# Kernel optimization log

Measured on AMD Instinct MI355X. Metric: run time of the kernel, lower is better.

The kernel has to match this reference:

```python
import jax, jax.numpy as jnp
import numpy as np

N_NODES = 50000
N_EDGES = 800000
NODE_F = 128
EDGE_F = 64
OUT_F = 128


def setup_inputs() -> dict:
    key = jax.random.key(0)
    k1, k2, k3, k4, k5 = jax.random.split(key, 5)
    x = jax.random.normal(k1, (N_NODES, NODE_F), dtype=jnp.float32)
    edge_index = jax.random.randint(k2, (2, N_EDGES), 0, N_NODES, dtype=jnp.int64)
    edge_attr = jax.random.normal(k3, (N_EDGES, EDGE_F), dtype=jnp.float32)
    # Linear(node_features + edge_features, out_features) params (torch default init scale)
    fan_in = NODE_F + EDGE_F
    bound = 1.0 / np.sqrt(fan_in)
    W = jax.random.uniform(k4, (fan_in, OUT_F), minval=-bound, maxval=bound, dtype=jnp.float32)
    b = jax.random.uniform(k5, (OUT_F,), minval=-bound, maxval=bound, dtype=jnp.float32)
    return {"x": x, "edge_index": edge_index, "edge_attr": edge_attr, "W": W, "b": b}


def reference(x, edge_index, edge_attr, W, b):
    # PyG source_to_target flow: x_j = x[src], aggregate at dst
    src = edge_index[0]
    dst = edge_index[1]
    x_j = x[src]                                   # [E, node_f] gather
    feats = jnp.concatenate([edge_attr, x_j], axis=1)  # [E, edge_f + node_f]
    msg = jax.nn.relu(feats @ W + b)               # [E, out_f] Linear + ReLU
    out = jax.ops.segment_sum(msg, dst, num_segments=x.shape[0])  # scatter-add
    return out
```

## Files before the change

kernel.cpp:

```cpp
#include <hip/hip_runtime.h>
#include <hip/hip_bf16.h>

#define N_NODES 50000
#define N_EDGES 800000
#define NODE_F  128
#define EDGE_F  64
#define OUT_F   128

#define NCH ((N_NODES + 255) / 256)
#define EPW 128
#define NRANGES (N_EDGES / EPW)

typedef __attribute__((ext_vector_type(8))) short short8;
typedef __attribute__((ext_vector_type(4))) short short4v;
typedef __attribute__((ext_vector_type(4))) float floatx4;

__device__ __forceinline__ unsigned short f2bf(float f) {
    unsigned int u = __float_as_uint(f);
    u += 0x7fffu + ((u >> 16) & 1u);
    return (unsigned short)(u >> 16);
}

__device__ __forceinline__ short8 cvt8(floatx4 v0, floatx4 v1) {
    union { __hip_bfloat162 h[4]; short8 s; } u;
    u.h[0] = __float22bfloat162_rn(make_float2(v0[0], v0[1]));
    u.h[1] = __float22bfloat162_rn(make_float2(v0[2], v0[3]));
    u.h[2] = __float22bfloat162_rn(make_float2(v1[0], v1[1]));
    u.h[3] = __float22bfloat162_rn(make_float2(v1[2], v1[3]));
    return u.s;
}

#define TILE_N1 32
#define N_NTILES ((N_NODES + TILE_N1 - 1) / TILE_N1)
#define LDS_STRIDE1 136

__global__ __launch_bounds__(256, 4) void node_kernel(
    const float* __restrict__ x,
    const float* __restrict__ W,
    const float* __restrict__ bias,
    float*       __restrict__ Y)
{
    __shared__ __align__(16) unsigned short xs[TILE_N1][LDS_STRIDE1];

    const int tid  = threadIdx.x;
    const int wave = tid >> 6;
    const int lane = tid & 63;
    const int col  = lane & 15;
    const int quad = lane >> 4;
    const int wbase = wave * 32;

    const float* __restrict__ Wx = W + EDGE_F * OUT_F;

    short8 bfr[4][2];
    #pragma unroll
    for (int kc = 0; kc < 4; ++kc) {
        #pragma unroll
        for (int ns = 0; ns < 2; ++ns) {
            const int n = wbase + ns * 16 + col;
            const int krow = kc * 32 + quad * 8;
            short8 v;
            #pragma unroll
            for (int j = 0; j < 8; ++j)
                v[j] = (short)f2bf(Wx[(krow + j) * OUT_F + n]);
            bfr[kc][ns] = v;
        }
    }
    const float b0 = bias[wbase + col];
    const float b1 = bias[wbase + 16 + col];

    for (int tile = blockIdx.x; tile < N_NTILES; tile += gridDim.x) {
        const int n0 = tile * TILE_N1;
        {
            const int e   = tid >> 3;
            const int sub = tid & 7;
            const int node = n0 + e;
            const float* __restrict__ xr = x + (size_t)node * NODE_F;
            #pragma unroll
            for (int i = 0; i < 4; ++i) {
                const int fi = sub + 8 * i;
                floatx4 v = {0.f, 0.f, 0.f, 0.f};
                if (node < N_NODES) v = *(const floatx4*)(xr + fi * 4);
                union { __hip_bfloat162 h[2]; short4v s; } u;
                u.h[0] = __float22bfloat162_rn(make_float2(v[0], v[1]));
                u.h[1] = __float22bfloat162_rn(make_float2(v[2], v[3]));
                *(short4v*)&xs[e][fi * 4] = u.s;
            }
        }
        __syncthreads();

        floatx4 acc[2][2] = {};
        #pragma unroll
        for (int kc = 0; kc < 4; ++kc) {
            short8 a0 = *(const short8*)&xs[col     ][kc * 32 + quad * 8];
            short8 a1 = *(const short8*)&xs[16 + col][kc * 32 + quad * 8];
            acc[0][0] = __builtin_amdgcn_mfma_f32_16x16x32_bf16(a0, bfr[kc][0], acc[0][0], 0, 0, 0);
            acc[0][1] = __builtin_amdgcn_mfma_f32_16x16x32_bf16(a0, bfr[kc][1], acc[0][1], 0, 0, 0);
            acc[1][0] = __builtin_amdgcn_mfma_f32_16x16x32_bf16(a1, bfr[kc][0], acc[1][0], 0, 0, 0);
            acc[1][1] = __builtin_amdgcn_mfma_f32_16x16x32_bf16(a1, bfr[kc][1], acc[1][1], 0, 0, 0);
        }

        #pragma unroll
        for (int ms = 0; ms < 2; ++ms) {
            #pragma unroll
            for (int r = 0; r < 4; ++r) {
                const int m = ms * 16 + quad * 4 + r;
                const int node = n0 + m;
                if (node < N_NODES) {
                    float* yrow = Y + (size_t)node * OUT_F + wbase;
                    yrow[col]      = acc[ms][0][r] + b0;
                    yrow[16 + col] = acc[ms][1][r] + b1;
                }
            }
        }
        __syncthreads();
    }
}

__global__ void hist_kernel(const int* __restrict__ edge_index, int* __restrict__ hist) {
    const int* dstp = edge_index + N_EDGES;
    for (int i = blockIdx.x * blockDim.x + threadIdx.x; i < N_EDGES;
         i += gridDim.x * blockDim.x)
        atomicAdd(&hist[dstp[i]], 1);
}

__global__ void scan1_kernel(const int* __restrict__ hist, int* __restrict__ chunkSum) {
    __shared__ int s[256];
    const int c = blockIdx.x, t = threadIdx.x, idx = c * 256 + t;
    s[t] = (idx < N_NODES) ? hist[idx] : 0;
    __syncthreads();
    for (int off = 128; off > 0; off >>= 1) {
        if (t < off) s[t] += s[t + off];
        __syncthreads();
    }
    if (t == 0) chunkSum[c] = s[0];
}

__global__ void scan2_kernel(const int* __restrict__ chunkSum, int* __restrict__ chunkBase) {
    __shared__ int s[256];
    const int t = threadIdx.x;
    s[t] = (t < NCH) ? chunkSum[t] : 0;
    __syncthreads();
    for (int off = 1; off < 256; off <<= 1) {
        int u = (t >= off) ? s[t - off] : 0;
        __syncthreads();
        s[t] += u;
        __syncthreads();
    }
    if (t < NCH) chunkBase[t] = (t == 0) ? 0 : s[t - 1];
}

__global__ void scan3_kernel(const int* __restrict__ hist, const int* __restrict__ chunkBase,
                             int* __restrict__ row_off, int* __restrict__ cursor) {
    __shared__ int s[256];
    const int c = blockIdx.x, t = threadIdx.x, idx = c * 256 + t;
    const int v = (idx < N_NODES) ? hist[idx] : 0;
    s[t] = v;
    __syncthreads();
    for (int off = 1; off < 256; off <<= 1) {
        int u = (t >= off) ? s[t - off] : 0;
        __syncthreads();
        s[t] += u;
        __syncthreads();
    }
    const int excl = s[t] - v + chunkBase[c];
    if (idx < N_NODES) { row_off[idx] = excl; cursor[idx] = excl; }
    if (c == 0 && t == 0) row_off[N_NODES] = N_EDGES;
}

__device__ __forceinline__ int lbound(const int* __restrict__ ro, int target) {
    int lo = 0, hi = N_NODES;
    while (lo < hi) {
        const int mid = (lo + hi) >> 1;
        if (ro[mid] < target) lo = mid + 1; else hi = mid;
    }
    return lo;
}

__global__ void range_kernel(const int* __restrict__ row_off, int* __restrict__ range_start) {
    const int rg = blockIdx.x * blockDim.x + threadIdx.x;
    if (rg <= NRANGES) range_start[rg] = row_off[lbound(row_off, rg * EPW)];
}

__global__ void scatter_kernel(const int* __restrict__ edge_index,
                               int* __restrict__ cursor, int2* __restrict__ sorted) {
    const int* srcp = edge_index;
    const int* dstp = edge_index + N_EDGES;
    for (int i = blockIdx.x * blockDim.x + threadIdx.x; i < N_EDGES;
         i += gridDim.x * blockDim.x) {
        const int d = dstp[i];
        const int p = atomicAdd(&cursor[d], 1);
        sorted[p] = make_int2(i, (int)(((unsigned)srcp[i] << 16) | (unsigned)d));
    }
}

__global__ __launch_bounds__(256, 6) void edge_gemm(
    const float* __restrict__ edge_attr,
    const float* __restrict__ W,
    const float* __restrict__ Y,
    const int*   __restrict__ range_start,
    const int2*  __restrict__ sorted,
    float*       __restrict__ out)
{
    __shared__ float CT[4][16][68];

    const int tid  = threadIdx.x;
    const int wave = tid >> 6;
    const int lane = tid & 63;
    const int col  = lane & 15;
    const int quad = lane >> 4;
    const int p    = wave & 1;

    short8 bfr[2][4];
    #pragma unroll
    for (int kc = 0; kc < 2; ++kc) {
        #pragma unroll
        for (int ns = 0; ns < 4; ++ns) {
            const int n = p * 64 + ns * 16 + col;
            const int krow = kc * 32 + quad * 8;
            short8 v;
            #pragma unroll
            for (int j = 0; j < 8; ++j)
                v[j] = (short)f2bf(W[(krow + j) * OUT_F + n]);
            bfr[kc][ns] = v;
        }
    }

    float* __restrict__ obase = out + p * 64 + lane;

    const int grange = blockIdx.x * 2 + (wave >> 1);
    const int stride = gridDim.x * 2;

    for (int rg = grange; rg < NRANGES; rg += stride) {
        const int eb = range_start[rg];
        const int ee = range_start[rg + 1];
        if (eb >= ee) continue;

        int   cur = -1;
        float s   = 0.f;

        int2 me = sorted[min(eb + col, ee - 1)];
        short8 a[2];
        {
            const float* __restrict__ ar = edge_attr + (size_t)me.x * EDGE_F;
            #pragma unroll
            for (int kc = 0; kc < 2; ++kc)
                a[kc] = cvt8(*(const floatx4*)(ar + kc * 32 + quad * 8),
                             *(const floatx4*)(ar + kc * 32 + quad * 8 + 4));
        }

        for (int t0 = eb; t0 < ee; t0 += 16) {
            floatx4 acc[4];
            #pragma unroll
            for (int r = 0; r < 4; ++r) {
                const int src = (int)((unsigned)__shfl(me.y, quad * 4 + r) >> 16);
                const float* __restrict__ yr = Y + (size_t)src * OUT_F + p * 64;
                #pragma unroll
                for (int ns = 0; ns < 4; ++ns)
                    acc[ns][r] = yr[ns * 16 + col];
            }

            #pragma unroll
            for (int kc = 0; kc < 2; ++kc) {
                #pragma unroll
                for (int ns = 0; ns < 4; ++ns)
                    acc[ns] = __builtin_amdgcn_mfma_f32_16x16x32_bf16(a[kc], bfr[kc][ns], acc[ns], 0, 0, 0);
            }

            #pragma unroll
            for (int r = 0; r < 4; ++r) {
                const bool rvalid = (t0 + quad * 4 + r) < ee;
                #pragma unroll
                for (int ns = 0; ns < 4; ++ns)
                    CT[wave][quad * 4 + r][ns * 16 + col] =
                        rvalid ? fmaxf(acc[ns][r], 0.f) : 0.f;
            }
            __builtin_amdgcn_wave_barrier();

            const int t1 = t0 + 16;
            int2 me2;
            if (t1 < ee) me2 = sorted[min(t1 + col, ee - 1)];

            float cv[16];
            #pragma unroll
            for (int m = 0; m < 16; ++m) cv[m] = CT[wave][m][lane];

            const int mez = me.y;
            #pragma unroll
            for (int m = 0; m < 16; ++m) {
                const int d = (int)((unsigned)__builtin_amdgcn_readlane(mez, m) & 0xffffu);
                if (d != cur) {
                    if (cur >= 0) obase[(size_t)cur * OUT_F] = s;
                    cur = d; s = 0.f;
                }
                s += cv[m];
            }
            cur = __builtin_amdgcn_readfirstlane(cur);
            __builtin_amdgcn_wave_barrier();

            if (t1 < ee) {
                me = me2;
                const float* __restrict__ ar = edge_attr + (size_t)me.x * EDGE_F;
                #pragma unroll
                for (int kc = 0; kc < 2; ++kc)
                    a[kc] = cvt8(*(const floatx4*)(ar + kc * 32 + quad * 8),
                                 *(const floatx4*)(ar + kc * 32 + quad * 8 + 4));
            }
        }
        if (cur >= 0) obase[(size_t)cur * OUT_F] = s;
    }
}

__global__ __launch_bounds__(256, 3) void edge_kernel_atomic(
    const float* __restrict__ edge_attr,
    const int*   __restrict__ edge_index,
    const float* __restrict__ W,
    const float* __restrict__ Y,
    float*       __restrict__ out)
{
    const int lane = threadIdx.x & 63;
    const int col  = lane & 15;
    const int quad = lane >> 4;

    short8 bfr[2][8];
    #pragma unroll
    for (int kc = 0; kc < 2; ++kc)
        #pragma unroll
        for (int ns = 0; ns < 8; ++ns) {
            const int n = ns * 16 + col;
            const int krow = kc * 32 + quad * 8;
            short8 v;
            #pragma unroll
            for (int j = 0; j < 8; ++j)
                v[j] = (short)f2bf(W[(krow + j) * OUT_F + n]);
            bfr[kc][ns] = v;
        }

    const int* __restrict__ srcp = edge_index;
    const int* __restrict__ dstp = edge_index + N_EDGES;

    const int gwave  = blockIdx.x * 4 + (threadIdx.x >> 6);
    const int nwaves = gridDim.x * 4;

    for (int t = gwave; t < N_EDGES / 16; t += nwaves) {
        const int e0 = t * 16;
        const float* __restrict__ ar = edge_attr + (size_t)(e0 + col) * EDGE_F;
        short8 a[2];
        #pragma unroll
        for (int kc = 0; kc < 2; ++kc)
            a[kc] = cvt8(*(const floatx4*)(ar + kc * 32 + quad * 8),
                         *(const floatx4*)(ar + kc * 32 + quad * 8 + 4));
        int sr[4], dr[4];
        #pragma unroll
        for (int r = 0; r < 4; ++r) {
            sr[r] = srcp[e0 + quad * 4 + r];
            dr[r] = dstp[e0 + quad * 4 + r];
        }
        floatx4 acc[8];
        #pragma unroll
        for (int ns = 0; ns < 8; ++ns)
            #pragma unroll
            for (int r = 0; r < 4; ++r)
                acc[ns][r] = Y[(size_t)sr[r] * OUT_F + ns * 16 + col];
        #pragma unroll
        for (int kc = 0; kc < 2; ++kc)
            #pragma unroll
            for (int ns = 0; ns < 8; ++ns)
                acc[ns] = __builtin_amdgcn_mfma_f32_16x16x32_bf16(a[kc], bfr[kc][ns], acc[ns], 0, 0, 0);
        #pragma unroll
        for (int ns = 0; ns < 8; ++ns)
            #pragma unroll
            for (int r = 0; r < 4; ++r) {
                const float v = acc[ns][r];
                if (v > 0.0f)
                    atomicAdd(out + (size_t)dr[r] * OUT_F + ns * 16 + col, v);
            }
    }
}

extern "C" void kernel_launch(void* const* d_in, const int* in_sizes, int n_in,
                              void* d_out, int out_size, void* d_ws, size_t ws_size,
                              hipStream_t stream) {
    const float* x          = (const float*)d_in[0];
    const int*   edge_index = (const int*)  d_in[1];
    const float* edge_attr  = (const float*)d_in[2];
    const float* W          = (const float*)d_in[3];
    const float* bias       = (const float*)d_in[4];
    float*       out        = (float*)d_out;

    float* Y          = (float*)d_ws;
    int2*  sorted     = (int2*)(Y + (size_t)N_NODES * OUT_F);
    int*   hist       = (int*)(sorted + N_EDGES);
    int*   chunkSum   = hist + N_NODES;
    int*   chunkBase  = chunkSum + 256;
    int*   row_off    = chunkBase + 256;
    int*   cursor     = row_off + N_NODES + 1;
    int*   range_start= cursor + N_NODES;
    const size_t needed = (size_t)((char*)(range_start + NRANGES + 1) - (char*)d_ws);

    hipMemsetAsync(out, 0, (size_t)out_size * sizeof(float), stream);
    node_kernel<<<dim3(512), dim3(256), 0, stream>>>(x, W, bias, Y);

    if (ws_size < needed) {
        edge_kernel_atomic<<<dim3(1024), dim3(256), 0, stream>>>(edge_attr, edge_index, W, Y, out);
        return;
    }

    hipMemsetAsync(hist, 0, (size_t)N_NODES * sizeof(int), stream);
    hist_kernel   <<<dim3(2048), dim3(256), 0, stream>>>(edge_index, hist);
    scan1_kernel  <<<dim3(NCH),  dim3(256), 0, stream>>>(hist, chunkSum);
    scan2_kernel  <<<dim3(1),    dim3(256), 0, stream>>>(chunkSum, chunkBase);
    scan3_kernel  <<<dim3(NCH),  dim3(256), 0, stream>>>(hist, chunkBase, row_off, cursor);
    range_kernel  <<<dim3((NRANGES + 256) / 256), dim3(256), 0, stream>>>(row_off, range_start);
    scatter_kernel<<<dim3(2048), dim3(256), 0, stream>>>(edge_index, cursor, sorted);
    edge_gemm     <<<dim3(1536), dim3(256), 0, stream>>>(
        edge_attr, W, Y, range_start, sorted, out);
}
```

Before: 483.8 us.

## Pre-convert edge features to bf16 and software-pipeline edge gather loads

Fuses the destination histogram with a pass that converts edge_attr to a bf16 workspace copy. The edge GEMM then reads half-width rows in sorted (random) order instead of converting fp32 on the fly. The main loop now prefetches the next tile's edge features and Y rows before the current tile's reduction, to overlap gather latency with MFMA and segment-sum work. This adds a full extra read and write pass over edge_attr and more register pressure (occupancy hint lowered to 5). The grid size is also adjusted.

```diff
diff --git a/kernel.cpp b/kernel.cpp
--- a/kernel.cpp
+++ b/kernel.cpp
@@ -28,6 +28,24 @@
     u.h[2] = __float22bfloat162_rn(make_float2(v1[0], v1[1]));
     u.h[3] = __float22bfloat162_rn(make_float2(v1[2], v1[3]));
     return u.s;
+}
+
+__global__ void prep_kernel(const float* __restrict__ edge_attr,
+                            const int*   __restrict__ edge_index,
+                            unsigned short* __restrict__ ea16,
+                            int* __restrict__ hist, int do_cvt) {
+    const int tid    = blockIdx.x * blockDim.x + threadIdx.x;
+    const int stride = gridDim.x * blockDim.x;
+    const int* dstp  = edge_index + N_EDGES;
+    for (int i = tid; i < N_EDGES; i += stride) atomicAdd(&hist[dstp[i]], 1);
+    if (do_cvt) {
+        const int nchunk = N_EDGES * EDGE_F / 8;
+        for (int i = tid; i < nchunk; i += stride) {
+            floatx4 v0 = *(const floatx4*)(edge_attr + (size_t)i * 8);
+            floatx4 v1 = *(const floatx4*)(edge_attr + (size_t)i * 8 + 4);
+            *(short8*)(ea16 + (size_t)i * 8) = cvt8(v0, v1);
+        }
+    }
 }
 
 #define TILE_N1 32
@@ -114,13 +132,6 @@
         }
         __syncthreads();
     }
-}
-
-__global__ void hist_kernel(const int* __restrict__ edge_index, int* __restrict__ hist) {
-    const int* dstp = edge_index + N_EDGES;
-    for (int i = blockIdx.x * blockDim.x + threadIdx.x; i < N_EDGES;
-         i += gridDim.x * blockDim.x)
-        atomicAdd(&hist[dstp[i]], 1);
 }
 
 __global__ void scan1_kernel(const int* __restrict__ hist, int* __restrict__ chunkSum) {
@@ -193,8 +204,10 @@
     }
 }
 
-__global__ __launch_bounds__(256, 6) void edge_gemm(
+template <bool EA16>
+__global__ __launch_bounds__(256, 5) void edge_gemm(
     const float* __restrict__ edge_attr,
+    const unsigned short* __restrict__ ea16,
     const float* __restrict__ W,
     const float* __restrict__ Y,
     const int*   __restrict__ range_start,
@@ -227,6 +240,31 @@
 
     float* __restrict__ obase = out + p * 64 + lane;
 
+    short8  a[2];
+    floatx4 yv[4];
+
+    auto load_a = [&](int eid) {
+        if constexpr (EA16) {
+            const unsigned short* __restrict__ r = ea16 + (size_t)eid * EDGE_F + quad * 8;
+            a[0] = *(const short8*)r;
+            a[1] = *(const short8*)(r + 32);
+        } else {
+            const float* __restrict__ ar = edge_attr + (size_t)eid * EDGE_F + quad * 8;
+            a[0] = cvt8(*(const floatx4*)ar,        *(const floatx4*)(ar + 4));
+            a[1] = cvt8(*(const floatx4*)(ar + 32), *(const floatx4*)(ar + 36));
+        }
+    };
+    auto gather_y = [&](int mey) {
+        #pragma unroll
+        for (int r = 0; r < 4; ++r) {
+            const int src = (int)((unsigned)__shfl(mey, quad * 4 + r) >> 16);
+            const float* __restrict__ yr = Y + (size_t)src * OUT_F + p * 64;
+            #pragma unroll
+            for (int ns = 0; ns < 4; ++ns)
+                yv[ns][r] = yr[ns * 16 + col];
+        }
+    };
+
     const int grange = blockIdx.x * 2 + (wave >> 1);
     const int stride = gridDim.x * 2;
 
@@ -239,32 +277,26 @@
         float s   = 0.f;
 
         int2 me = sorted[min(eb + col, ee - 1)];
-        short8 a[2];
-        {
-            const float* __restrict__ ar = edge_attr + (size_t)me.x * EDGE_F;
-            #pragma unroll
-            for (int kc = 0; kc < 2; ++kc)
-                a[kc] = cvt8(*(const floatx4*)(ar + kc * 32 + quad * 8),
-                             *(const floatx4*)(ar + kc * 32 + quad * 8 + 4));
-        }
+        load_a(me.x);
+        gather_y(me.y);
 
         for (int t0 = eb; t0 < ee; t0 += 16) {
+            const int  t1   = t0 + 16;
+            const bool more = t1 < ee;
+            int2 me2;
+            if (more) me2 = sorted[min(t1 + col, ee - 1)];
+
             floatx4 acc[4];
             #pragma unroll
-            for (int r = 0; r < 4; ++r) {
-                const int src = (int)((unsigned)__shfl(me.y, quad * 4 + r) >> 16);
-                const float* __restrict__ yr = Y + (size_t)src * OUT_F + p * 64;
-                #pragma unroll
-                for (int ns = 0; ns < 4; ++ns)
-                    acc[ns][r] = yr[ns * 16 + col];
-            }
-
+            for (int ns = 0; ns < 4; ++ns) acc[ns] = yv[ns];
             #pragma unroll
             for (int kc = 0; kc < 2; ++kc) {
                 #pragma unroll
                 for (int ns = 0; ns < 4; ++ns)
                     acc[ns] = __builtin_amdgcn_mfma_f32_16x16x32_bf16(a[kc], bfr[kc][ns], acc[ns], 0, 0, 0);
             }
+
+            if (more) { load_a(me2.x); gather_y(me2.y); }
 
             #pragma unroll
             for (int r = 0; r < 4; ++r) {
@@ -275,10 +307,6 @@
                         rvalid ? fmaxf(acc[ns][r], 0.f) : 0.f;
             }
             __builtin_amdgcn_wave_barrier();
-
-            const int t1 = t0 + 16;
-            int2 me2;
-            if (t1 < ee) me2 = sorted[min(t1 + col, ee - 1)];
 
             float cv[16];
             #pragma unroll
@@ -297,14 +325,7 @@
             cur = __builtin_amdgcn_readfirstlane(cur);
             __builtin_amdgcn_wave_barrier();
 
-            if (t1 < ee) {
-                me = me2;
-                const float* __restrict__ ar = edge_attr + (size_t)me.x * EDGE_F;
-                #pragma unroll
-                for (int kc = 0; kc < 2; ++kc)
-                    a[kc] = cvt8(*(const floatx4*)(ar + kc * 32 + quad * 8),
-                                 *(const floatx4*)(ar + kc * 32 + quad * 8 + 4));
-            }
+            if (more) me = me2;
         }
         if (cur >= 0) obase[(size_t)cur * OUT_F] = s;
     }
@@ -395,23 +416,33 @@
     int*   row_off    = chunkBase + 256;
     int*   cursor     = row_off + N_NODES + 1;
     int*   range_start= cursor + N_NODES;
-    const size_t needed = (size_t)((char*)(range_start + NRANGES + 1) - (char*)d_ws);
+    size_t off16 = ((size_t)((char*)(range_start + NRANGES + 1) - (char*)d_ws) + 15) & ~(size_t)15;
+    unsigned short* ea16 = (unsigned short*)((char*)d_ws + off16);
+    const size_t needed_b = off16;
+    const size_t needed_a = off16 + (size_t)N_EDGES * EDGE_F * sizeof(unsigned short);
 
     hipMemsetAsync(out, 0, (size_t)out_size * sizeof(float), stream);
-    node_kernel<<<dim3(512), dim3(256), 0, stream>>>(x, W, bias, Y);
-
-    if (ws_size < needed) {
+
+    if (ws_size < needed_b) {
+        node_kernel<<<dim3(512), dim3(256), 0, stream>>>(x, W, bias, Y);
         edge_kernel_atomic<<<dim3(1024), dim3(256), 0, stream>>>(edge_attr, edge_index, W, Y, out);
         return;
     }
 
+    const int use16 = (ws_size >= needed_a) ? 1 : 0;
+
     hipMemsetAsync(hist, 0, (size_t)N_NODES * sizeof(int), stream);
-    hist_kernel   <<<dim3(2048), dim3(256), 0, stream>>>(edge_index, hist);
+    prep_kernel   <<<dim3(1024), dim3(256), 0, stream>>>(edge_attr, edge_index, ea16, hist, use16);
+    node_kernel   <<<dim3(512),  dim3(256), 0, stream>>>(x, W, bias, Y);
     scan1_kernel  <<<dim3(NCH),  dim3(256), 0, stream>>>(hist, chunkSum);
     scan2_kernel  <<<dim3(1),    dim3(256), 0, stream>>>(chunkSum, chunkBase);
     scan3_kernel  <<<dim3(NCH),  dim3(256), 0, stream>>>(hist, chunkBase, row_off, cursor);
     range_kernel  <<<dim3((NRANGES + 256) / 256), dim3(256), 0, stream>>>(row_off, range_start);
     scatter_kernel<<<dim3(2048), dim3(256), 0, stream>>>(edge_index, cursor, sorted);
-    edge_gemm     <<<dim3(1536), dim3(256), 0, stream>>>(
-        edge_attr, W, Y, range_start, sorted, out);
-}
+    if (use16)
+        edge_gemm<true><<<dim3(1563), dim3(256), 0, stream>>>(
+            edge_attr, ea16, W, Y, range_start, sorted, out);
+    else
+        edge_gemm<false><<<dim3(1563), dim3(256), 0, stream>>>(
+            edge_attr, ea16, W, Y, range_start, sorted, out);
+}
```

After: 558.6 us. 1.15x slower.
